# Performance work log

Hardware: AMD Instinct MI355X
Metric: run time of the kernel (lower is better)

## Reference

```python
import jax, jax.numpy as jnp
import numpy as np

H = 8          # num_heads
D = 64         # head_dim
HID = 512      # hidden_size
W = 128        # window_size
NEG = -1e9

def setup_inputs() -> dict:
    key = jax.random.key(0)
    ks = jax.random.split(key, 12)
    B, S = 2, 2048
    def lin(i):
        w = jax.random.normal(ks[i], (HID, HID), dtype=jnp.float32) * (1.0 / np.sqrt(HID))
        b = jax.random.normal(ks[i + 1], (HID,), dtype=jnp.float32) * 0.01
        return w, b
    Wq, bq = lin(0)
    Wk, bk = lin(2)
    Wv, bv = lin(4)
    Wo, bo = lin(6)
    return {
        "value": jax.random.normal(ks[8], (B, S, HID), dtype=jnp.float32),
        "key": jax.random.normal(ks[9], (B, S, HID), dtype=jnp.float32),
        "query": jax.random.normal(ks[10], (B, S, HID), dtype=jnp.float32),
        "Wq": Wq, "bq": bq, "Wk": Wk, "bk": bk,
        "Wv": Wv, "bv": bv, "Wo": Wo, "bo": bo,
    }

def reference(value, key, query, Wq, bq, Wk, bk, Wv, bv, Wo, bo):
    B, S, _ = query.shape
    def heads(x, Wt, b):
        # torch Linear: x @ W.T + b ; then [B,S,H,D] -> [B,H,S,D]
        return (x @ Wt.T + b).reshape(B, S, H, D).transpose(0, 2, 1, 3)
    Q = heads(query, Wq, bq)
    K = heads(key, Wk, bk)
    V = heads(value, Wv, bv)
    scores = jnp.einsum('bhqd,bhkd->bhqk', Q, K) / jnp.sqrt(jnp.float32(D))
    idx = jnp.arange(S)
    local = jnp.abs(idx[:, None] - idx[None, :]) <= W  # [S,S] band mask
    scores = jnp.where(local[None, None], scores, NEG)
    weights = jax.nn.softmax(scores, axis=-1)
    out = jnp.einsum('bhqk,bhkd->bhqd', weights, V)
    out = out.transpose(0, 2, 1, 3).reshape(B, S, HID)
    return out @ Wo.T + bo
```

## Files before the change

kernel.cpp:

```cpp
#include <hip/hip_runtime.h>
#include <stdint.h>

#define B_   2
#define S_   2048
#define H_   8
#define D_   64
#define HID_ 512
#define W_   128
#define M_   (B_ * S_)
#define E_   (M_ * HID_)
#define PPAD_ 72
#define M0_  12.0f

typedef unsigned short u16;
typedef __attribute__((ext_vector_type(8))) __bf16 bf16x8;
typedef __attribute__((ext_vector_type(4))) float  floatx4;

__device__ __forceinline__ u16 f2b(float f) {
    union { __bf16 b; u16 u; } x;
    x.b = (__bf16)f;
    return x.u;
}

__device__ __forceinline__ void gll16(const u16* g, u16* l) {
    __builtin_amdgcn_global_load_lds(
        (const __attribute__((address_space(1))) unsigned int*)g,
        (__attribute__((address_space(3))) unsigned int*)l, 16, 0, 0);
}

__device__ __forceinline__ void cvt8_store(float4 a, float4 b, u16* dst) {
    bf16x8 v;
    v[0] = (__bf16)a.x; v[1] = (__bf16)a.y; v[2] = (__bf16)a.z; v[3] = (__bf16)a.w;
    v[4] = (__bf16)b.x; v[5] = (__bf16)b.y; v[6] = (__bf16)b.z; v[7] = (__bf16)b.w;
    *(bf16x8*)dst = v;
}

__device__ __forceinline__ void frag_mfma(const u16* As, const u16* Bs,
                                          const int aoff[2], const int boff[2],
                                          floatx4 acc[4][4]) {
    bf16x8 af[2][4], bf[2][4];
#pragma unroll
    for (int ks = 0; ks < 2; ks++)
#pragma unroll
        for (int t = 0; t < 4; t++) {
            af[ks][t] = *(const bf16x8*)&As[aoff[ks] + t * 1024];
            bf[ks][t] = *(const bf16x8*)&Bs[boff[ks] + t * 1024];
        }
#pragma unroll
    for (int ks = 0; ks < 2; ks++)
#pragma unroll
        for (int i = 0; i < 4; i++)
#pragma unroll
            for (int j = 0; j < 4; j++)
                acc[i][j] = __builtin_amdgcn_mfma_f32_16x16x32_bf16(
                    af[ks][i], bf[ks][j], acc[i][j], 0, 0, 0);
}

template <int MODE>
__device__ __forceinline__ void gemm_qkv(
    const float* __restrict__ Xf, const float* __restrict__ Wf,
    const float* __restrict__ bias, u16* __restrict__ outH,
    u16* As, u16* Bs, int m0, int n0) {
    const int tid  = threadIdx.x;
    const int wave = tid >> 6;
    const int lane = tid & 63;
    const int r16  = lane & 15;
    const int quad = lane >> 4;
    const int mq = (wave >> 1) * 64;
    const int nq = (wave & 1) * 64;

    floatx4 zero = {0.f, 0.f, 0.f, 0.f};
    floatx4 acc[4][4];
#pragma unroll
    for (int i = 0; i < 4; i++)
#pragma unroll
        for (int j = 0; j < 4; j++) acc[i][j] = zero;

    int aoff[2], boff[2];
#pragma unroll
    for (int ks = 0; ks < 2; ks++) {
        const int sw = (((ks * 4 + quad) ^ (r16 & 7)) * 8);
        aoff[ks] = (mq + r16) * 64 + sw;
        boff[ks] = (nq + r16) * 64 + sw;
    }

    const float* Xa = Xf + (size_t)m0 * HID_;
    const float* Wb = Wf + (size_t)n0 * HID_;
    float4 pa[8], pb[8];

#define QLOAD(dst, Base, k0) do {                                              \
        _Pragma("unroll")                                                      \
        for (int e = 0; e < 4; e++) {                                          \
            const int slot = e * 256 + tid;                                    \
            const int r_ = slot >> 3, c_ = slot & 7;                           \
            const float4* s_ = (const float4*)(Base + (size_t)r_ * HID_ + (k0) + c_ * 8); \
            dst[2 * e] = s_[0]; dst[2 * e + 1] = s_[1];                        \
        }                                                                      \
    } while (0)

    QLOAD(pa, Xa, 0);
    QLOAD(pb, Wb, 0);

    for (int k0 = 0; k0 < HID_; k0 += 64) {
        __syncthreads();
#pragma unroll
        for (int e = 0; e < 4; e++) {
            const int slot = e * 256 + tid;
            const int r_ = slot >> 3, c_ = slot & 7;
            const int sw = r_ * 64 + ((c_ ^ (r_ & 7)) * 8);
            cvt8_store(pa[2 * e], pa[2 * e + 1], &As[sw]);
            cvt8_store(pb[2 * e], pb[2 * e + 1], &Bs[sw]);
        }
        __syncthreads();
        if (k0 + 64 < HID_) {
            QLOAD(pa, Xa, k0 + 64);
            QLOAD(pb, Wb, k0 + 64);
        }
        frag_mfma(As, Bs, aoff, boff, acc);
    }
#undef QLOAD

    const int m_base = m0 + mq;
    const int bb = m_base >> 11;
    if (MODE == 1) {
#pragma unroll
        for (int j = 0; j < 4; j++) {
            const int col = n0 + nq + j * 16 + r16;
            const int h = col >> 6, d = col & (D_ - 1);
            const float bv = bias[col];
            const size_t base = (size_t)(bb * H_ + h) * S_;
#pragma unroll
            for (int i = 0; i < 4; i++)
#pragma unroll
                for (int r = 0; r < 4; r++) {
                    const int s = (m_base & (S_ - 1)) + i * 16 + quad * 4 + r;
                    outH[(base + s) * D_ + d] = f2b(acc[i][j][r] + bv);
                }
        }
    } else {
#pragma unroll
        for (int j = 0; j < 4; j++) {
            const int col = n0 + nq + j * 16 + r16;
            const int h = col >> 6, d = col & (D_ - 1);
            const float bv = bias[col];
            const size_t base = ((size_t)(bb * H_ + h) * D_ + d) * S_;
            const int s0 = (m_base & (S_ - 1)) + quad * 4;
#pragma unroll
            for (int i = 0; i < 4; i++) {
                ushort4 hs;
                hs.x = f2b(acc[i][j][0] + bv);
                hs.y = f2b(acc[i][j][1] + bv);
                hs.z = f2b(acc[i][j][2] + bv);
                hs.w = f2b(acc[i][j][3] + bv);
                *(ushort4*)(outH + base + s0 + i * 16) = hs;
            }
        }
    }
}

__global__ __launch_bounds__(256) void qkv_kernel(
    const float* __restrict__ xq, const float* __restrict__ xk, const float* __restrict__ xv,
    const float* __restrict__ wq, const float* __restrict__ wk, const float* __restrict__ wv,
    const float* __restrict__ bq, const float* __restrict__ bk, const float* __restrict__ bv,
    u16* __restrict__ P) {
    __shared__ u16 As[128 * 64];
    __shared__ u16 Bs[128 * 64];
    const int m0 = blockIdx.x * 128, n0 = blockIdx.y * 128;
    const int z = blockIdx.z;
    if (z == 0)      gemm_qkv<1>(xq, wq, bq, P,                    As, Bs, m0, n0);
    else if (z == 1) gemm_qkv<1>(xk, wk, bk, P + E_,               As, Bs, m0, n0);
    else             gemm_qkv<2>(xv, wv, bv, P + 2 * (size_t)E_,   As, Bs, m0, n0);
}

__global__ __launch_bounds__(256) void out_kernel(
    const u16* __restrict__ AOh, const float* __restrict__ Wf,
    const float* __restrict__ bias, float* __restrict__ outF) {
    __shared__ u16 As[128 * 64];
    __shared__ u16 Bs[128 * 64];

    const int tid  = threadIdx.x;
    const int wave = tid >> 6;
    const int lane = tid & 63;
    const int r16  = lane & 15;
    const int quad = lane >> 4;
    const int m0 = blockIdx.x * 128, n0 = blockIdx.y * 128;
    const int mq = (wave >> 1) * 64;
    const int nq = (wave & 1) * 64;

    floatx4 zero = {0.f, 0.f, 0.f, 0.f};
    floatx4 acc[4][4];
#pragma unroll
    for (int i = 0; i < 4; i++)
#pragma unroll
        for (int j = 0; j < 4; j++) acc[i][j] = zero;

    int aoff[2], boff[2];
#pragma unroll
    for (int ks = 0; ks < 2; ks++) {
        const int sw = (((ks * 4 + quad) ^ (r16 & 7)) * 8);
        aoff[ks] = (mq + r16) * 64 + sw;
        boff[ks] = (nq + r16) * 64 + sw;
    }

    const float* Wb = Wf + (size_t)n0 * HID_;
    float4 pb[8];
#define OLOADB(k0) do {                                                        \
        _Pragma("unroll")                                                      \
        for (int e = 0; e < 4; e++) {                                          \
            const int slot = e * 256 + tid;                                    \
            const int r_ = slot >> 3, c_ = slot & 7;                           \
            const float4* s_ = (const float4*)(Wb + (size_t)r_ * HID_ + (k0) + c_ * 8); \
            pb[2 * e] = s_[0]; pb[2 * e + 1] = s_[1];                          \
        }                                                                      \
    } while (0)

    OLOADB(0);
    for (int k0 = 0; k0 < HID_; k0 += 64) {
        __syncthreads();
#pragma unroll
        for (int e = 0; e < 4; e++) {
            const int li = (wave * 4 + e) * 64 + lane;
            const int r_ = li >> 3;
            const int cl = (li & 7) ^ (r_ & 7);
            gll16(AOh + (size_t)(m0 + r_) * HID_ + k0 + cl * 8,
                  As + (size_t)(wave * 4 + e) * 512);
        }
#pragma unroll
        for (int e = 0; e < 4; e++) {
            const int slot = e * 256 + tid;
            const int r_ = slot >> 3, c_ = slot & 7;
            cvt8_store(pb[2 * e], pb[2 * e + 1], &Bs[r_ * 64 + ((c_ ^ (r_ & 7)) * 8)]);
        }
        __syncthreads();
        if (k0 + 64 < HID_) OLOADB(k0 + 64);
        frag_mfma(As, Bs, aoff, boff, acc);
    }
#undef OLOADB

    const int m_base = m0 + mq;
#pragma unroll
    for (int j = 0; j < 4; j++) {
        const int col = n0 + nq + j * 16 + r16;
        const float bv = bias[col];
#pragma unroll
        for (int i = 0; i < 4; i++) {
            const int row0 = m_base + i * 16 + quad * 4;
#pragma unroll
            for (int r = 0; r < 4; r++)
                outF[(size_t)(row0 + r) * HID_ + col] = acc[i][j][r] + bv;
        }
    }
}

__global__ __launch_bounds__(256) void attn_kernel(
    const u16* __restrict__ Qh, const u16* __restrict__ Kh,
    const u16* __restrict__ Vth, u16* __restrict__ AOh) {
    __shared__ u16 Ps[4][16][PPAD_];
    __shared__ u16 Osh[4][16][PPAD_];

    const int tid  = threadIdx.x;
    const int wave = tid >> 6;
    const int lane = tid & 63;
    const int r16 = lane & 15, quad = lane >> 4;
    u16* Psw  = &Ps[wave][0][0];
    u16* Oshw = &Osh[wave][0][0];

    const int qt = blockIdx.x & 31, bh = blockIdx.x >> 5;
    const int q0 = qt * 64 + wave * 16;
    const size_t sd = (size_t)bh * S_ * D_;
    const size_t ds = (size_t)bh * D_ * S_;

    bf16x8 qf[2];
#pragma unroll
    for (int ks = 0; ks < 2; ks++)
        qf[ks] = *(const bf16x8*)(Qh + sd + (size_t)(q0 + r16) * D_ + ks * 32 + quad * 8);

    floatx4 zero = {0.f, 0.f, 0.f, 0.f};
    floatx4 O[4];
    float lsum[4];
#pragma unroll
    for (int j = 0; j < 4; j++) O[j] = zero;
#pragma unroll
    for (int r = 0; r < 4; r++) lsum[r] = 0.f;

    int t_lo = qt - 2; if (t_lo < 0) t_lo = 0;
    int t_hi = qt + 2; if (t_hi > S_ / 64 - 1) t_hi = S_ / 64 - 1;

    for (int t = t_lo; t <= t_hi; ++t) {
        const int k0 = t * 64;
        floatx4 sa[4];
#pragma unroll
        for (int j = 0; j < 4; j++) sa[j] = zero;

#pragma unroll
        for (int ks = 0; ks < 2; ks++) {
            bf16x8 kf[4];
#pragma unroll
            for (int j = 0; j < 4; j++)
                kf[j] = *(const bf16x8*)(Kh + sd + (size_t)(k0 + j * 16 + r16) * D_ + ks * 32 + quad * 8);
#pragma unroll
            for (int j = 0; j < 4; j++)
                sa[j] = __builtin_amdgcn_mfma_f32_16x16x32_bf16(qf[ks], kf[j], sa[j], 0, 0, 0);
        }

#pragma unroll
        for (int j = 0; j < 4; j++) {
            const int kc = k0 + j * 16 + r16;
#pragma unroll
            for (int r = 0; r < 4; r++) {
                const int q = q0 + quad * 4 + r;
                const bool valid = (unsigned)(kc - q + W_) <= (unsigned)(2 * W_);
                const float p = valid ? __expf(fmaf(sa[j][r], 0.125f, -M0_)) : 0.f;
                lsum[r] += p;
                Psw[(quad * 4 + r) * PPAD_ + j * 16 + r16] = f2b(p);
            }
        }

#pragma unroll
        for (int ks = 0; ks < 2; ks++) {
            bf16x8 pf = *(const bf16x8*)&Psw[r16 * PPAD_ + ks * 32 + quad * 8];
#pragma unroll
            for (int j = 0; j < 4; j++) {
                bf16x8 vf = *(const bf16x8*)(Vth + ds + (size_t)(j * 16 + r16) * S_ + k0 + ks * 32 + quad * 8);
                O[j] = __builtin_amdgcn_mfma_f32_16x16x32_bf16(pf, vf, O[j], 0, 0, 0);
            }
        }
    }

#pragma unroll
    for (int r = 0; r < 4; r++) {
        float l = lsum[r];
#pragma unroll
        for (int off = 1; off < 16; off <<= 1) l += __shfl_xor(l, off, 64);
        lsum[r] = l;
    }

#pragma unroll
    for (int r = 0; r < 4; r++) {
        const float linv = 1.f / lsum[r];
#pragma unroll
        for (int j = 0; j < 4; j++)
            Oshw[(quad * 4 + r) * PPAD_ + j * 16 + r16] = f2b(O[j][r] * linv);
    }

    const int b = bh >> 3, h = bh & 7;
    const int qq = lane >> 2;
    const int d0 = (lane & 3) * 16;
    u16* dst = AOh + (size_t)(b * S_ + q0 + qq) * HID_ + h * D_ + d0;
    *(uint4*)dst       = *(const uint4*)&Oshw[qq * PPAD_ + d0];
    *(uint4*)(dst + 8) = *(const uint4*)&Oshw[qq * PPAD_ + d0 + 8];
}

extern "C" void kernel_launch(void* const* d_in, const int* in_sizes, int n_in,
                              void* d_out, int out_size, void* d_ws, size_t ws_size,
                              hipStream_t stream) {
    const float* value = (const float*)d_in[0];
    const float* key_  = (const float*)d_in[1];
    const float* query = (const float*)d_in[2];
    const float* Wq = (const float*)d_in[3];
    const float* bq = (const float*)d_in[4];
    const float* Wk = (const float*)d_in[5];
    const float* bk = (const float*)d_in[6];
    const float* Wv = (const float*)d_in[7];
    const float* bv = (const float*)d_in[8];
    const float* Wo = (const float*)d_in[9];
    const float* bo = (const float*)d_in[10];

    u16* P   = (u16*)d_ws;
    u16* AOh = P + 3 * (size_t)E_;

    qkv_kernel<<<dim3(M_ / 128, HID_ / 128, 3), 256, 0, stream>>>(
        query, key_, value, Wq, Wk, Wv, bq, bk, bv, P);
    attn_kernel<<<dim3((S_ / 64) * B_ * H_), 256, 0, stream>>>(
        P, P + E_, P + 2 * (size_t)E_, AOh);
    out_kernel<<<dim3(M_ / 128, HID_ / 128), 256, 0, stream>>>(
        AOh, Wo, bo, (float*)d_out);
}
```

Before: 143.6 us.

## Double-buffer LDS tiles in QKV and output GEMMs to overlap loads with MFMA

Both projection GEMMs now keep two LDS buffers for the A and B tiles. The next K-slice is loaded and stored into the spare buffer while MFMAs run on the current one, which leaves one barrier per iteration instead of two. The attention kernel moves to a 2D grid and indexes shared arrays directly, which looks like a cosmetic change. Shared memory per block doubles, and that may reduce occupancy.

```diff
diff --git a/kernel.cpp b/kernel.cpp
--- a/kernel.cpp
+++ b/kernel.cpp
@@ -60,7 +60,7 @@
 __device__ __forceinline__ void gemm_qkv(
     const float* __restrict__ Xf, const float* __restrict__ Wf,
     const float* __restrict__ bias, u16* __restrict__ outH,
-    u16* As, u16* Bs, int m0, int n0) {
+    u16* As0, u16* As1, u16* Bs0, u16* Bs1, int m0, int n0) {
     const int tid  = threadIdx.x;
     const int wave = tid >> 6;
     const int lane = tid & 63;
@@ -97,28 +97,40 @@
             dst[2 * e] = s_[0]; dst[2 * e + 1] = s_[1];                        \
         }                                                                      \
     } while (0)
+#define QSTORE(src, Dst) do {                                                  \
+        _Pragma("unroll")                                                      \
+        for (int e = 0; e < 4; e++) {                                          \
+            const int slot = e * 256 + tid;                                    \
+            const int r_ = slot >> 3, c_ = slot & 7;                           \
+            cvt8_store(src[2 * e], src[2 * e + 1],                             \
+                       Dst + r_ * 64 + ((c_ ^ (r_ & 7)) * 8));                 \
+        }                                                                      \
+    } while (0)
 
     QLOAD(pa, Xa, 0);
     QLOAD(pb, Wb, 0);
-
-    for (int k0 = 0; k0 < HID_; k0 += 64) {
+    QSTORE(pa, As0);
+    QSTORE(pb, Bs0);
+    __syncthreads();
+
+    u16 *Ac = As0, *Bc = Bs0, *An = As1, *Bn = Bs1;
+    for (int t = 0; t < 8; t++) {
+        if (t < 7) {
+            QLOAD(pa, Xa, (t + 1) * 64);
+            QLOAD(pb, Wb, (t + 1) * 64);
+        }
+        frag_mfma(Ac, Bc, aoff, boff, acc);
+        if (t < 7) {
+            QSTORE(pa, An);
+            QSTORE(pb, Bn);
+        }
         __syncthreads();
-#pragma unroll
-        for (int e = 0; e < 4; e++) {
-            const int slot = e * 256 + tid;
-            const int r_ = slot >> 3, c_ = slot & 7;
-            const int sw = r_ * 64 + ((c_ ^ (r_ & 7)) * 8);
-            cvt8_store(pa[2 * e], pa[2 * e + 1], &As[sw]);
-            cvt8_store(pb[2 * e], pb[2 * e + 1], &Bs[sw]);
-        }
-        __syncthreads();
-        if (k0 + 64 < HID_) {
-            QLOAD(pa, Xa, k0 + 64);
-            QLOAD(pb, Wb, k0 + 64);
-        }
-        frag_mfma(As, Bs, aoff, boff, acc);
+        u16* tp;
+        tp = Ac; Ac = An; An = tp;
+        tp = Bc; Bc = Bn; Bn = tp;
     }
 #undef QLOAD
+#undef QSTORE
 
     const int m_base = m0 + mq;
     const int bb = m_base >> 11;
@@ -163,20 +175,23 @@
     const float* __restrict__ wq, const float* __restrict__ wk, const float* __restrict__ wv,
     const float* __restrict__ bq, const float* __restrict__ bk, const float* __restrict__ bv,
     u16* __restrict__ P) {
-    __shared__ u16 As[128 * 64];
-    __shared__ u16 Bs[128 * 64];
+    __shared__ u16 As[2][128 * 64];
+    __shared__ u16 Bs[2][128 * 64];
     const int m0 = blockIdx.x * 128, n0 = blockIdx.y * 128;
     const int z = blockIdx.z;
-    if (z == 0)      gemm_qkv<1>(xq, wq, bq, P,                    As, Bs, m0, n0);
-    else if (z == 1) gemm_qkv<1>(xk, wk, bk, P + E_,               As, Bs, m0, n0);
-    else             gemm_qkv<2>(xv, wv, bv, P + 2 * (size_t)E_,   As, Bs, m0, n0);
+    if (z == 0)
+        gemm_qkv<1>(xq, wq, bq, P,                  As[0], As[1], Bs[0], Bs[1], m0, n0);
+    else if (z == 1)
+        gemm_qkv<1>(xk, wk, bk, P + E_,             As[0], As[1], Bs[0], Bs[1], m0, n0);
+    else
+        gemm_qkv<2>(xv, wv, bv, P + 2 * (size_t)E_, As[0], As[1], Bs[0], Bs[1], m0, n0);
 }
 
 __global__ __launch_bounds__(256) void out_kernel(
     const u16* __restrict__ AOh, const float* __restrict__ Wf,
     const float* __restrict__ bias, float* __restrict__ outF) {
-    __shared__ u16 As[128 * 64];
-    __shared__ u16 Bs[128 * 64];
+    __shared__ u16 As[2][128 * 64];
+    __shared__ u16 Bs[2][128 * 64];
 
     const int tid  = threadIdx.x;
     const int wave = tid >> 6;
@@ -204,6 +219,17 @@
 
     const float* Wb = Wf + (size_t)n0 * HID_;
     float4 pb[8];
+
+#define OSTAGEA(kk, Ad) do {                                                   \
+        _Pragma("unroll")                                                      \
+        for (int e = 0; e < 4; e++) {                                          \
+            const int li = (wave * 4 + e) * 64 + lane;                         \
+            const int r_ = li >> 3;                                            \
+            const int cl = (li & 7) ^ (r_ & 7);                                \
+            gll16(AOh + (size_t)(m0 + r_) * HID_ + (kk) + cl * 8,              \
+                  Ad + (size_t)(wave * 4 + e) * 512);                          \
+        }                                                                      \
+    } while (0)
 #define OLOADB(k0) do {                                                        \
         _Pragma("unroll")                                                      \
         for (int e = 0; e < 4; e++) {                                          \
@@ -213,29 +239,37 @@
             pb[2 * e] = s_[0]; pb[2 * e + 1] = s_[1];                          \
         }                                                                      \
     } while (0)
-
+#define OSTOREB(Bd) do {                                                       \
+        _Pragma("unroll")                                                      \
+        for (int e = 0; e < 4; e++) {                                          \
+            const int slot = e * 256 + tid;                                    \
+            const int r_ = slot >> 3, c_ = slot & 7;                           \
+            cvt8_store(pb[2 * e], pb[2 * e + 1],                               \
+                       Bd + r_ * 64 + ((c_ ^ (r_ & 7)) * 8));                  \
+        }                                                                      \
+    } while (0)
+
+    OSTAGEA(0, As[0]);
     OLOADB(0);
-    for (int k0 = 0; k0 < HID_; k0 += 64) {
+    OSTOREB(Bs[0]);
+    __syncthreads();
+
+    u16 *Ac = As[0], *Bc = Bs[0], *An = As[1], *Bn = Bs[1];
+    for (int t = 0; t < 8; t++) {
+        if (t < 7) {
+            OSTAGEA((t + 1) * 64, An);
+            OLOADB((t + 1) * 64);
+        }
+        frag_mfma(Ac, Bc, aoff, boff, acc);
+        if (t < 7) OSTOREB(Bn);
         __syncthreads();
-#pragma unroll
-        for (int e = 0; e < 4; e++) {
-            const int li = (wave * 4 + e) * 64 + lane;
-            const int r_ = li >> 3;
-            const int cl = (li & 7) ^ (r_ & 7);
-            gll16(AOh + (size_t)(m0 + r_) * HID_ + k0 + cl * 8,
-                  As + (size_t)(wave * 4 + e) * 512);
-        }
-#pragma unroll
-        for (int e = 0; e < 4; e++) {
-            const int slot = e * 256 + tid;
-            const int r_ = slot >> 3, c_ = slot & 7;
-            cvt8_store(pb[2 * e], pb[2 * e + 1], &Bs[r_ * 64 + ((c_ ^ (r_ & 7)) * 8)]);
-        }
-        __syncthreads();
-        if (k0 + 64 < HID_) OLOADB(k0 + 64);
-        frag_mfma(As, Bs, aoff, boff, acc);
-    }
+        u16* tp;
+        tp = Ac; Ac = An; An = tp;
+        tp = Bc; Bc = Bn; Bn = tp;
+    }
+#undef OSTAGEA
 #undef OLOADB
+#undef OSTOREB
 
     const int m_base = m0 + mq;
 #pragma unroll
@@ -262,10 +296,7 @@
     const int wave = tid >> 6;
     const int lane = tid & 63;
     const int r16 = lane & 15, quad = lane >> 4;
-    u16* Psw  = &Ps[wave][0][0];
-    u16* Oshw = &Osh[wave][0][0];
-
-    const int qt = blockIdx.x & 31, bh = blockIdx.x >> 5;
+    const int qt = blockIdx.x, bh = blockIdx.y;
     const int q0 = qt * 64 + wave * 16;
     const size_t sd = (size_t)bh * S_ * D_;
     const size_t ds = (size_t)bh * D_ * S_;
@@ -312,13 +343,13 @@
                 const bool valid = (unsigned)(kc - q + W_) <= (unsigned)(2 * W_);
                 const float p = valid ? __expf(fmaf(sa[j][r], 0.125f, -M0_)) : 0.f;
                 lsum[r] += p;
-                Psw[(quad * 4 + r) * PPAD_ + j * 16 + r16] = f2b(p);
+                Ps[wave][quad * 4 + r][j * 16 + r16] = f2b(p);
             }
         }
 
 #pragma unroll
         for (int ks = 0; ks < 2; ks++) {
-            bf16x8 pf = *(const bf16x8*)&Psw[r16 * PPAD_ + ks * 32 + quad * 8];
+            bf16x8 pf = *(const bf16x8*)&Ps[wave][r16][ks * 32 + quad * 8];
 #pragma unroll
             for (int j = 0; j < 4; j++) {
                 bf16x8 vf = *(const bf16x8*)(Vth + ds + (size_t)(j * 16 + r16) * S_ + k0 + ks * 32 + quad * 8);
@@ -340,15 +371,15 @@
         const float linv = 1.f / lsum[r];
 #pragma unroll
         for (int j = 0; j < 4; j++)
-            Oshw[(quad * 4 + r) * PPAD_ + j * 16 + r16] = f2b(O[j][r] * linv);
+            Osh[wave][quad * 4 + r][j * 16 + r16] = f2b(O[j][r] * linv);
     }
 
     const int b = bh >> 3, h = bh & 7;
     const int qq = lane >> 2;
     const int d0 = (lane & 3) * 16;
     u16* dst = AOh + (size_t)(b * S_ + q0 + qq) * HID_ + h * D_ + d0;
-    *(uint4*)dst       = *(const uint4*)&Oshw[qq * PPAD_ + d0];
-    *(uint4*)(dst + 8) = *(const uint4*)&Oshw[qq * PPAD_ + d0 + 8];
+    *(uint4*)dst       = *(const uint4*)&Osh[wave][qq][d0];
+    *(uint4*)(dst + 8) = *(const uint4*)&Osh[wave][qq][d0 + 8];
 }
 
 extern "C" void kernel_launch(void* const* d_in, const int* in_sizes, int n_in,
@@ -371,7 +402,7 @@
 
     qkv_kernel<<<dim3(M_ / 128, HID_ / 128, 3), 256, 0, stream>>>(
         query, key_, value, Wq, Wk, Wv, bq, bk, bv, P);
-    attn_kernel<<<dim3((S_ / 64) * B_ * H_), 256, 0, stream>>>(
+    attn_kernel<<<dim3(S_ / 64, B_ * H_), 256, 0, stream>>>(
         P, P + E_, P + 2 * (size_t)E_, AOh);
     out_kernel<<<dim3(M_ / 128, HID_ / 128), 256, 0, stream>>>(
         AOh, Wo, bo, (float*)d_out);
```

New measurement: 141.5 us. Within noise of the previous version (-1.5%).
